# Kernel optimization log

Measured on AMD Instinct MI355X. Metric: run time of the kernel, lower is better.

## Reference

```python
import jax, jax.numpy as jnp
import numpy as np

B, S, IN, H, D, STATE, PRED = 256, 512, 32, 256, 32, 4, 96


def setup_inputs() -> dict:
    key = jax.random.key(0)
    ks = jax.random.split(key, 16)
    sc = 1.0 / np.sqrt(H)

    def u(k, shape):
        return jax.random.uniform(k, shape, jnp.float32, -sc, sc)

    return {
        "x": jax.random.normal(ks[0], (B, S, IN), jnp.float32),
        # GRU layer 0
        "W_ih_l0": u(ks[1], (3 * H, IN)),
        "W_hh_l0": u(ks[2], (3 * H, H)),
        "b_ih_l0": u(ks[3], (3 * H,)),
        "b_hh_l0": u(ks[4], (3 * H,)),
        # GRU layer 1
        "W_ih_l1": u(ks[5], (3 * H, H)),
        "W_hh_l1": u(ks[6], (3 * H, H)),
        "b_ih_l1": u(ks[7], (3 * H,)),
        "b_hh_l1": u(ks[8], (3 * H,)),
        # state projection: hidden -> STATE*output_dim
        "W_proj": u(ks[9], (STATE * D, H)),
        "b_proj": u(ks[10], (STATE * D,)),
        # observation matrix, eye-initialized (output_dim, STATE)
        "C": jnp.eye(D, STATE, dtype=jnp.float32),
        "raw_level_decay": jnp.zeros((D,), jnp.float32),
        "raw_trend_decay": jnp.zeros((D,), jnp.float32),
        "raw_gamma": jnp.zeros((D,), jnp.float32),
        "omega": jnp.zeros((D,), jnp.float32),
    }


def _gru_layer(xs, W_ih, W_hh, b_ih, b_hh):
    # xs: (B, S, in_dim). Precompute input projections as one big GEMM.
    xp = jnp.einsum('bsi,gi->bsg', xs, W_ih) + b_ih  # (B, S, 3H)

    def step(h, xt):
        gh = h @ W_hh.T + b_hh  # (B, 3H)
        xr, xz, xn = jnp.split(xt, 3, axis=-1)
        hr, hz, hn = jnp.split(gh, 3, axis=-1)
        r = jax.nn.sigmoid(xr + hr)
        z = jax.nn.sigmoid(xz + hz)
        n = jnp.tanh(xn + r * hn)
        h_new = (1.0 - z) * n + z * h
        return h_new, h_new

    h0 = jnp.zeros((xs.shape[0], W_hh.shape[1]), xs.dtype)
    _, hs = jax.lax.scan(step, h0, jnp.swapaxes(xp, 0, 1))  # (S, B, H)
    return jnp.swapaxes(hs, 0, 1)  # (B, S, H)


def reference(x, W_ih_l0, W_hh_l0, b_ih_l0, b_hh_l0,
              W_ih_l1, W_hh_l1, b_ih_l1, b_hh_l1,
              W_proj, b_proj, C,
              raw_level_decay, raw_trend_decay, raw_gamma, omega):
    h1 = _gru_layer(x, W_ih_l0, W_hh_l0, b_ih_l0, b_hh_l0)
    h2 = _gru_layer(h1, W_ih_l1, W_hh_l1, b_ih_l1, b_hh_l1)
    final_h = h2[:, -1, :]  # (B, H)

    d_out = C.shape[0]
    s = (final_h @ W_proj.T + b_proj).reshape(x.shape[0], d_out, STATE)  # (B, D, 4)

    # time-invariant block-diagonal transition coefficients
    a_l = jax.nn.sigmoid(raw_level_decay) * 0.15 + 0.85
    a_t = jax.nn.sigmoid(raw_trend_decay) * 0.25 + 0.7
    g = jax.nn.sigmoid(raw_gamma) * 0.2 + 0.8
    c, sn = jnp.cos(omega), jnp.sin(omega)
    rot00, rot01 = g * c, -g * sn
    rot10, rot11 = g * sn, g * c

    def step(s, _):
        new_s = jnp.stack([
            s[..., 0] * a_l,
            s[..., 1] * a_t,
            s[..., 2] * rot00 + s[..., 3] * rot10,
            s[..., 2] * rot01 + s[..., 3] * rot11,
        ], axis=-1)
        y = jnp.einsum('ds,bds->bd', C, new_s)
        return new_s, y

    _, ys = jax.lax.scan(step, s, None, length=PRED)  # (PRED, B, D)
    return jnp.swapaxes(ys, 0, 1)  # (B, PRED, D)
```

## Files before the change

### kernel.cpp

```cpp
#include <hip/hip_runtime.h>
#include <cstdio>
#include <cstdint>

typedef _Float16 f16;
typedef f16 hf2   __attribute__((ext_vector_type(2)));
typedef f16 f16x8 __attribute__((ext_vector_type(8)));
typedef float f32x4 __attribute__((ext_vector_type(4)));
typedef unsigned int   u32;
typedef unsigned short u16;

#define B_    256
#define S_    512
#define IN_   32
#define H_    256
#define G3_   768
#define D_    32
#define PRED_ 96
#define TC_   32
#define XPAD_ 776

#if __has_builtin(__builtin_amdgcn_fdot2)
__device__ __forceinline__ float fdot2(hf2 a, hf2 b, float c) {
  return __builtin_amdgcn_fdot2(a, b, c, false);
}
#else
__device__ __forceinline__ float fdot2(hf2 a, hf2 b, float c) {
  return c + (float)a[0] * (float)b[0] + (float)a[1] * (float)b[1];
}
#endif

__device__ __forceinline__ float sigm(float x) {
  return __builtin_amdgcn_rcpf(1.f + __expf(-x));
}
__device__ __forceinline__ float tanh_fast(float x) {
  return 1.f - 2.f * __builtin_amdgcn_rcpf(__expf(2.f * x) + 1.f);
}
__device__ __forceinline__ hf2 bc2(u32 v) { return __builtin_bit_cast(hf2, v); }

__global__ void f32_to_f16_k(const float* __restrict__ in, f16* __restrict__ out, int n) {
  int i = blockIdx.x * blockDim.x + threadIdx.x;
  if (i < n) out[i] = (f16)in[i];
}

__device__ __forceinline__ f16x8 cvt8(const float* p) {
  float4 lo = ((const float4*)p)[0];
  float4 hi = ((const float4*)p)[1];
  f16x8 r;
  r[0] = (f16)lo.x; r[1] = (f16)lo.y; r[2] = (f16)lo.z; r[3] = (f16)lo.w;
  r[4] = (f16)hi.x; r[5] = (f16)hi.y; r[6] = (f16)hi.z; r[7] = (f16)hi.w;
  return r;
}

template <int LAYER>
__global__ __launch_bounds__(512, 1) void gru_fused(
    const void* __restrict__ Asrc,
    const f16* __restrict__ Wih,
    const float* __restrict__ bih,
    const float* __restrict__ Whh,
    const float* __restrict__ bhh,
    f16* __restrict__ h16_out,
    float* __restrict__ hfinal) {
  constexpr int KK = LAYER ? H_ : IN_;
  const int b   = blockIdx.x;
  const int tid = threadIdx.x;
  const int p  = tid >> 1, kh = tid & 1;
  const int wv = tid >> 6, lane = tid & 63, lm = lane & 15, q = lane >> 4;

  hf2 w[3][64];
#pragma unroll
  for (int g = 0; g < 3; g++) {
    const float4* src = (const float4*)(Whh + (size_t)(g * 256 + p) * 256 + kh * 128);
#pragma unroll
    for (int u = 0; u < 32; u++) {
      float4 f = src[u];
      w[g][2 * u]     = hf2{(f16)f.x, (f16)f.y};
      w[g][2 * u + 1] = hf2{(f16)f.z, (f16)f.w};
    }
  }
  float bh[3];
#pragma unroll
  for (int g = 0; g < 3; g++) bh[g] = bhh[g * 256 + p];

  __shared__ u16 xpc[TC_ * XPAD_];
  __shared__ __align__(16) u16 hbuf[2][256];
  if (tid < 128) ((u32*)hbuf[0])[tid] = 0u;
  float h = 0.f;
  f16* h16p = (LAYER == 0) ? (h16_out + (size_t)b * S_ * H_) : nullptr;
  int cur = 0;

  for (int c = 0; c < S_ / TC_; ++c) {
    const int t0 = c * TC_;
#pragma unroll 1
    for (int nt = 0; nt < 6; ++nt) {
      const int n0 = wv * 96 + nt * 16;
      const f16* Bp = Wih + (size_t)(n0 + lm) * KK + q * 8;
      f32x4 ac0 = {0.f, 0.f, 0.f, 0.f}, ac1 = ac0;
#pragma unroll
      for (int k0 = 0; k0 < KK; k0 += 32) {
        f16x8 bv = *(const f16x8*)(Bp + k0);
        f16x8 a0, a1;
        if constexpr (LAYER == 0) {
          const float* xr = (const float*)Asrc + ((size_t)b * S_ + t0 + lm) * IN_ + k0 + q * 8;
          a0 = cvt8(xr);
          a1 = cvt8(xr + 16 * IN_);
        } else {
          const f16* ar = (const f16*)Asrc + ((size_t)b * S_ + t0 + lm) * H_ + k0 + q * 8;
          a0 = *(const f16x8*)ar;
          a1 = *(const f16x8*)(ar + 16 * H_);
        }
        ac0 = __builtin_amdgcn_mfma_f32_16x16x32_f16(a0, bv, ac0, 0, 0, 0);
        ac1 = __builtin_amdgcn_mfma_f32_16x16x32_f16(a1, bv, ac1, 0, 0, 0);
      }
      const float bb = bih[n0 + lm];
#pragma unroll
      for (int r = 0; r < 4; ++r) {
        xpc[(q * 4 + r) * XPAD_ + n0 + lm]      = __builtin_bit_cast(u16, (f16)(ac0[r] + bb));
        xpc[(16 + q * 4 + r) * XPAD_ + n0 + lm] = __builtin_bit_cast(u16, (f16)(ac1[r] + bb));
      }
    }
    __syncthreads();

    for (int tl = 0; tl < TC_; ++tl) {
      float ar = 0.f, az = 0.f, an = 0.f, ar2 = 0.f, az2 = 0.f, an2 = 0.f;
      const uint4* hb = (const uint4*)hbuf[cur] + kh * 16;
#pragma unroll
      for (int cc = 0; cc < 16; ++cc) {
        uint4 hv = hb[cc];
        hf2 h0 = bc2(hv.x), h1 = bc2(hv.y), h2v = bc2(hv.z), h3 = bc2(hv.w);
        ar  = fdot2(w[0][4 * cc],     h0,  ar);
        ar2 = fdot2(w[0][4 * cc + 1], h1,  ar2);
        ar  = fdot2(w[0][4 * cc + 2], h2v, ar);
        ar2 = fdot2(w[0][4 * cc + 3], h3,  ar2);
        az  = fdot2(w[1][4 * cc],     h0,  az);
        az2 = fdot2(w[1][4 * cc + 1], h1,  az2);
        az  = fdot2(w[1][4 * cc + 2], h2v, az);
        az2 = fdot2(w[1][4 * cc + 3], h3,  az2);
        an  = fdot2(w[2][4 * cc],     h0,  an);
        an2 = fdot2(w[2][4 * cc + 1], h1,  an2);
        an  = fdot2(w[2][4 * cc + 2], h2v, an);
        an2 = fdot2(w[2][4 * cc + 3], h3,  an2);
      }
      ar += ar2; az += az2; an += an2;
      ar += __shfl_xor(ar, 1);
      az += __shfl_xor(az, 1);
      an += __shfl_xor(an, 1);

      const u16* xrow = xpc + tl * XPAD_;
      float xr = (float)__builtin_bit_cast(f16, xrow[p]);
      float xz = (float)__builtin_bit_cast(f16, xrow[256 + p]);
      float xn = (float)__builtin_bit_cast(f16, xrow[512 + p]);
      float r = sigm(xr + ar + bh[0]);
      float z = sigm(xz + az + bh[1]);
      float n = tanh_fast(xn + r * (an + bh[2]));
      h = (1.f - z) * n + z * h;

      if (kh == 0) {
        hbuf[cur ^ 1][p] = __builtin_bit_cast(u16, (f16)h);
        if constexpr (LAYER == 0) h16p[(size_t)(t0 + tl) * H_ + p] = (f16)h;
      }
      __syncthreads();
      cur ^= 1;
    }
  }
  if constexpr (LAYER == 1) {
    if (kh == 0) hfinal[b * H_ + p] = h;
  }
}

__global__ __launch_bounds__(128) void proj_rollout(
    const float* __restrict__ hfinal, const float* __restrict__ Wp,
    const float* __restrict__ bp, const float* __restrict__ Cm,
    const float* __restrict__ rld, const float* __restrict__ rtd,
    const float* __restrict__ rg, const float* __restrict__ om,
    float* __restrict__ out) {
  const int b = blockIdx.x, tid = threadIdx.x;
  __shared__ float fh[256];
  __shared__ float sb[128];
  ((float2*)fh)[tid] = ((const float2*)(hfinal + b * 256))[tid];
  __syncthreads();
  const float4* wrow = (const float4*)(Wp + tid * 256);
  float acc = 0.f;
#pragma unroll 16
  for (int k4 = 0; k4 < 64; k4++) {
    float4 wv = wrow[k4];
    acc += wv.x * fh[4 * k4] + wv.y * fh[4 * k4 + 1] + wv.z * fh[4 * k4 + 2] +
           wv.w * fh[4 * k4 + 3];
  }
  sb[tid] = acc + bp[tid];
  __syncthreads();
  if (tid < 32) {
    const int dd = tid;
    float s0 = sb[dd * 4], s1 = sb[dd * 4 + 1], s2 = sb[dd * 4 + 2], s3 = sb[dd * 4 + 3];
    float al = sigm(rld[dd]) * 0.15f + 0.85f;
    float at = sigm(rtd[dd]) * 0.25f + 0.70f;
    float g  = sigm(rg[dd]) * 0.20f + 0.80f;
    float cw = cosf(om[dd]), sw = sinf(om[dd]);
    float r00 = g * cw, r01 = -g * sw, r10 = g * sw, r11 = g * cw;
    float c0 = Cm[dd * 4], c1 = Cm[dd * 4 + 1], c2 = Cm[dd * 4 + 2], c3 = Cm[dd * 4 + 3];
    float* op = out + (size_t)b * PRED_ * D_ + dd;
    for (int t = 0; t < PRED_; t++) {
      float n0 = s0 * al, n1 = s1 * at;
      float n2 = s2 * r00 + s3 * r10;
      float n3 = s2 * r01 + s3 * r11;
      op[(size_t)t * D_] = c0 * n0 + c1 * n1 + c2 * n2 + c3 * n3;
      s0 = n0; s1 = n1; s2 = n2; s3 = n3;
    }
  }
}

extern "C" void kernel_launch(void* const* d_in, const int* in_sizes, int n_in,
                              void* d_out, int out_size, void* d_ws,
                              size_t ws_size, hipStream_t stream) {
  (void)in_sizes; (void)n_in; (void)out_size;
  const float* x     = (const float*)d_in[0];
  const float* Wih0  = (const float*)d_in[1];
  const float* Whh0  = (const float*)d_in[2];
  const float* bih0  = (const float*)d_in[3];
  const float* bhh0  = (const float*)d_in[4];
  const float* Wih1  = (const float*)d_in[5];
  const float* Whh1  = (const float*)d_in[6];
  const float* bih1  = (const float*)d_in[7];
  const float* bhh1  = (const float*)d_in[8];
  const float* Wproj = (const float*)d_in[9];
  const float* bproj = (const float*)d_in[10];
  const float* Cm    = (const float*)d_in[11];
  const float* rld   = (const float*)d_in[12];
  const float* rtd   = (const float*)d_in[13];
  const float* rg    = (const float*)d_in[14];
  const float* om    = (const float*)d_in[15];
  float* out = (float*)d_out;

  char* ws = (char*)d_ws;
  const size_t wi0_off = 0;
  const size_t wi1_off = 49152;
  const size_t h16_off = 442368;
  const size_t hf_off  = 67551232;
  const size_t need    = 67813376;
  if (ws_size < need) {
    fprintf(stderr, "kernel_launch: ws too small: have %zu need %zu — skipping\n",
            ws_size, need);
    return;
  }
  f16* wi016  = (f16*)(ws + wi0_off);
  f16* wi116  = (f16*)(ws + wi1_off);
  f16* h16    = (f16*)(ws + h16_off);
  float* hfin = (float*)(ws + hf_off);

  f32_to_f16_k<<<96, 256, 0, stream>>>(Wih0, wi016, G3_ * IN_);
  f32_to_f16_k<<<768, 256, 0, stream>>>(Wih1, wi116, G3_ * H_);
  gru_fused<0><<<B_, 512, 0, stream>>>((const void*)x,   wi016, bih0, Whh0, bhh0, h16, nullptr);
  gru_fused<1><<<B_, 512, 0, stream>>>((const void*)h16, wi116, bih1, Whh1, bhh1, nullptr, hfin);
  proj_rollout<<<B_, 128, 0, stream>>>(hfin, Wproj, bproj, Cm, rld, rtd, rg, om, out);
}
```

Baseline: 1.599 ms.

## Split GRU recurrent dot product across four threads per hidden unit

Doubles the GRU block to 1024 threads so each hidden unit's recurrent matvec is split four ways instead of two. This halves per-thread weight registers and serial fdot2 chain length, with a two-stage shuffle reduction. The shared h buffer is padded into 72-element segments to avoid LDS bank conflicts from the new access pattern. The input-projection MFMA work is redistributed over 16 waves. It risks more barrier cost per timestep, more shuffles, and longer dependent fdot2 chains now that the dual accumulators are dropped.

```diff
diff --git a/kernel.cpp b/kernel.cpp
--- a/kernel.cpp
+++ b/kernel.cpp
@@ -52,7 +52,7 @@
 }
 
 template <int LAYER>
-__global__ __launch_bounds__(512, 1) void gru_fused(
+__global__ __launch_bounds__(1024, 1) void gru_fused(
     const void* __restrict__ Asrc,
     const f16* __restrict__ Wih,
     const float* __restrict__ bih,
@@ -63,15 +63,15 @@
   constexpr int KK = LAYER ? H_ : IN_;
   const int b   = blockIdx.x;
   const int tid = threadIdx.x;
-  const int p  = tid >> 1, kh = tid & 1;
+  const int p  = tid >> 2, kq = tid & 3;
   const int wv = tid >> 6, lane = tid & 63, lm = lane & 15, q = lane >> 4;
 
-  hf2 w[3][64];
+  hf2 w[3][32];
 #pragma unroll
   for (int g = 0; g < 3; g++) {
-    const float4* src = (const float4*)(Whh + (size_t)(g * 256 + p) * 256 + kh * 128);
-#pragma unroll
-    for (int u = 0; u < 32; u++) {
+    const float4* src = (const float4*)(Whh + (size_t)(g * 256 + p) * 256 + kq * 64);
+#pragma unroll
+    for (int u = 0; u < 16; u++) {
       float4 f = src[u];
       w[g][2 * u]     = hf2{(f16)f.x, (f16)f.y};
       w[g][2 * u + 1] = hf2{(f16)f.z, (f16)f.w};
@@ -82,8 +82,8 @@
   for (int g = 0; g < 3; g++) bh[g] = bhh[g * 256 + p];
 
   __shared__ u16 xpc[TC_ * XPAD_];
-  __shared__ __align__(16) u16 hbuf[2][256];
-  if (tid < 128) ((u32*)hbuf[0])[tid] = 0u;
+  __shared__ __align__(16) u16 hbuf[2][288];
+  if (tid < 144) ((u32*)hbuf[0])[tid] = 0u;
   float h = 0.f;
   f16* h16p = (LAYER == 0) ? (h16_out + (size_t)b * S_ * H_) : nullptr;
   int cur = 0;
@@ -91,11 +91,11 @@
   for (int c = 0; c < S_ / TC_; ++c) {
     const int t0 = c * TC_;
 #pragma unroll 1
-    for (int nt = 0; nt < 6; ++nt) {
-      const int n0 = wv * 96 + nt * 16;
+    for (int nt = 0; nt < 3; ++nt) {
+      const int n0 = wv * 48 + nt * 16;
       const f16* Bp = Wih + (size_t)(n0 + lm) * KK + q * 8;
       f32x4 ac0 = {0.f, 0.f, 0.f, 0.f}, ac1 = ac0;
-#pragma unroll
+#pragma unroll 2
       for (int k0 = 0; k0 < KK; k0 += 32) {
         f16x8 bv = *(const f16x8*)(Bp + k0);
         f16x8 a0, a1;
@@ -121,29 +121,28 @@
     __syncthreads();
 
     for (int tl = 0; tl < TC_; ++tl) {
-      float ar = 0.f, az = 0.f, an = 0.f, ar2 = 0.f, az2 = 0.f, an2 = 0.f;
-      const uint4* hb = (const uint4*)hbuf[cur] + kh * 16;
-#pragma unroll
-      for (int cc = 0; cc < 16; ++cc) {
+      float ar = 0.f, az = 0.f, an = 0.f;
+      const uint4* hb = (const uint4*)hbuf[cur] + kq * 9;
+#pragma unroll
+      for (int cc = 0; cc < 8; ++cc) {
         uint4 hv = hb[cc];
         hf2 h0 = bc2(hv.x), h1 = bc2(hv.y), h2v = bc2(hv.z), h3 = bc2(hv.w);
-        ar  = fdot2(w[0][4 * cc],     h0,  ar);
-        ar2 = fdot2(w[0][4 * cc + 1], h1,  ar2);
-        ar  = fdot2(w[0][4 * cc + 2], h2v, ar);
-        ar2 = fdot2(w[0][4 * cc + 3], h3,  ar2);
-        az  = fdot2(w[1][4 * cc],     h0,  az);
-        az2 = fdot2(w[1][4 * cc + 1], h1,  az2);
-        az  = fdot2(w[1][4 * cc + 2], h2v, az);
-        az2 = fdot2(w[1][4 * cc + 3], h3,  az2);
-        an  = fdot2(w[2][4 * cc],     h0,  an);
-        an2 = fdot2(w[2][4 * cc + 1], h1,  an2);
-        an  = fdot2(w[2][4 * cc + 2], h2v, an);
-        an2 = fdot2(w[2][4 * cc + 3], h3,  an2);
-      }
-      ar += ar2; az += az2; an += an2;
-      ar += __shfl_xor(ar, 1);
-      az += __shfl_xor(az, 1);
-      an += __shfl_xor(an, 1);
+        ar = fdot2(w[0][4 * cc],     h0,  ar);
+        az = fdot2(w[1][4 * cc],     h0,  az);
+        an = fdot2(w[2][4 * cc],     h0,  an);
+        ar = fdot2(w[0][4 * cc + 1], h1,  ar);
+        az = fdot2(w[1][4 * cc + 1], h1,  az);
+        an = fdot2(w[2][4 * cc + 1], h1,  an);
+        ar = fdot2(w[0][4 * cc + 2], h2v, ar);
+        az = fdot2(w[1][4 * cc + 2], h2v, az);
+        an = fdot2(w[2][4 * cc + 2], h2v, an);
+        ar = fdot2(w[0][4 * cc + 3], h3,  ar);
+        az = fdot2(w[1][4 * cc + 3], h3,  az);
+        an = fdot2(w[2][4 * cc + 3], h3,  an);
+      }
+      ar += __shfl_xor(ar, 1); ar += __shfl_xor(ar, 2);
+      az += __shfl_xor(az, 1); az += __shfl_xor(az, 2);
+      an += __shfl_xor(an, 1); an += __shfl_xor(an, 2);
 
       const u16* xrow = xpc + tl * XPAD_;
       float xr = (float)__builtin_bit_cast(f16, xrow[p]);
@@ -154,8 +153,8 @@
       float n = tanh_fast(xn + r * (an + bh[2]));
       h = (1.f - z) * n + z * h;
 
-      if (kh == 0) {
-        hbuf[cur ^ 1][p] = __builtin_bit_cast(u16, (f16)h);
+      if (kq == 0) {
+        hbuf[cur ^ 1][(p >> 6) * 72 + (p & 63)] = __builtin_bit_cast(u16, (f16)h);
         if constexpr (LAYER == 0) h16p[(size_t)(t0 + tl) * H_ + p] = (f16)h;
       }
       __syncthreads();
@@ -163,7 +162,7 @@
     }
   }
   if constexpr (LAYER == 1) {
-    if (kh == 0) hfinal[b * H_ + p] = h;
+    if (kq == 0) hfinal[b * H_ + p] = h;
   }
 }
 
@@ -248,7 +247,7 @@
 
   f32_to_f16_k<<<96, 256, 0, stream>>>(Wih0, wi016, G3_ * IN_);
   f32_to_f16_k<<<768, 256, 0, stream>>>(Wih1, wi116, G3_ * H_);
-  gru_fused<0><<<B_, 512, 0, stream>>>((const void*)x,   wi016, bih0, Whh0, bhh0, h16, nullptr);
-  gru_fused<1><<<B_, 512, 0, stream>>>((const void*)h16, wi116, bih1, Whh1, bhh1, nullptr, hfin);
+  gru_fused<0><<<B_, 1024, 0, stream>>>((const void*)x,   wi016, bih0, Whh0, bhh0, h16, nullptr);
+  gru_fused<1><<<B_, 1024, 0, stream>>>((const void*)h16, wi116, bih1, Whh1, bhh1, nullptr, hfin);
   proj_rollout<<<B_, 128, 0, stream>>>(hfin, Wproj, bproj, Cm, rld, rtd, rg, om, out);
 }
```

Result: slower. 2.077 ms (+29.9%).
